# Performance work log

Hardware: AMD Instinct MI355X
Metric: run time of the kernel (lower is better)

The kernel has to match this reference:

```python
import jax, jax.numpy as jnp
import numpy as np

BS, T, H = 4, 2048, 512
N_HEAD = 8
D_HEAD = H // N_HEAD  # 64


def setup_inputs() -> dict:
    key = jax.random.key(0)
    k1, k2, k3 = jax.random.split(key, 3)
    x = jax.random.normal(k1, (BS, T, H), dtype=jnp.float32)
    # torch Linear(hidden, (2*n_head+1)*d_head) -> store transposed for x @ W
    w_qkv = jax.random.normal(k2, (H, (2 * N_HEAD + 1) * D_HEAD), dtype=jnp.float32) * (H ** -0.5)
    w_out = jax.random.normal(k3, (D_HEAD, H), dtype=jnp.float32) * (D_HEAD ** -0.5)
    return {"x": x, "w_qkv": w_qkv, "w_out": w_out}


def reference(x, w_qkv, w_out):
    bs, t, h = x.shape
    n_head, d_head = N_HEAD, D_HEAD
    scale = d_head ** -0.5

    qkv = x @ w_qkv  # [bs, t, (2*n_head+1)*d_head]
    q, k, v = jnp.split(qkv, [n_head * d_head, 2 * n_head * d_head], axis=-1)
    q = q.reshape(bs, t, n_head, d_head)
    k = k.reshape(bs, t, n_head, d_head)
    # v stays [bs, t, d_head]: a single V shared across all heads

    # causal mask: -inf strictly above the diagonal
    mask = jnp.triu(jnp.full((t, t), -jnp.inf, dtype=x.dtype), 1)

    # scores: [bs, n_head, t_q, t_k]
    attn_score = jnp.einsum('bqhd,bkhd->bhqk', q, k) * scale + mask
    attn_prob = jax.nn.softmax(attn_score, axis=-1)

    # shared V broadcast over heads: [bs, n_head, t, d_head]
    attn_vec = jnp.einsum('bhqk,bkd->bhqd', attn_prob, v)
    m_attn_vec = jnp.mean(attn_vec, axis=1)  # mean over heads -> [bs, t, d_head]

    out = m_attn_vec @ w_out  # [bs, t, hidden]
    return out, attn_prob
```

## Files before the change

### kernel.cpp

```cpp
#include <hip/hip_runtime.h>

typedef unsigned short u16;
typedef __bf16 bf16x8 __attribute__((ext_vector_type(8)));
typedef float f32x4 __attribute__((ext_vector_type(4)));
static_assert(sizeof(bf16x8) == 16, "bf16x8 must be 16B");

#define MFMA(a, b, c) __builtin_amdgcn_mfma_f32_16x16x32_bf16(a, b, c, 0, 0, 0)

__device__ __forceinline__ u16 f2bf(float f) {
  unsigned u = __float_as_uint(f);
  u += 0x7fffu + ((u >> 16) & 1u);
  return (u16)(u >> 16);
}

__global__ __launch_bounds__(256) void prep_kernel(
    const float* __restrict__ x, const float* __restrict__ wqkv,
    const float* __restrict__ wout, u16* __restrict__ xh,
    u16* __restrict__ wt, u16* __restrict__ wot) {
  int blk = blockIdx.x, tid = threadIdx.x;
  if (blk < 4096) {
    int idx = (blk * 256 + tid) * 4;
    float4 v = *(const float4*)(x + idx);
    ushort4 o;
    o.x = f2bf(v.x); o.y = f2bf(v.y); o.z = f2bf(v.z); o.w = f2bf(v.w);
    *(ushort4*)(xh + idx) = o;
  } else if (blk < 4096 + 2176) {
    int idx = (blk - 4096) * 256 + tid;
    int n = idx >> 9, k = idx & 511;
    float v = wqkv[k * 1088 + n];
    if (n < 512) v *= 0.125f;
    wt[idx] = f2bf(v);
  } else {
    int idx = (blk - 6272) * 256 + tid;
    int n = idx >> 6, d = idx & 63;
    wot[idx] = f2bf(wout[d * 512 + n]);
  }
}

__global__ __launch_bounds__(256) void qkv_gemm_kernel(
    const u16* __restrict__ xh, const u16* __restrict__ wt,
    u16* __restrict__ Qb, u16* __restrict__ Kb, u16* __restrict__ Vt) {
  __shared__ u16 As[128][40];
  __shared__ u16 Bs[64][40];
  const int tid = threadIdx.x;
  const int w = tid >> 6, l = tid & 63, g = l >> 4, c16 = l & 15;
  const int n0 = blockIdx.x * 64;
  const int m0 = blockIdx.y * 128;
  const int arow = tid >> 1, acol = (tid & 1) << 4;
  const int brow = tid >> 2, bcol = (tid & 3) << 3;
  const u16* ap = xh + (size_t)(m0 + arow) * 512 + acol;
  const u16* bp = wt + (size_t)(n0 + brow) * 512 + bcol;
  uint4 pa0 = *(const uint4*)(ap);
  uint4 pa1 = *(const uint4*)(ap + 8);
  uint4 pb0 = *(const uint4*)(bp);
  f32x4 acc[2][4] = {};
  for (int k0 = 0; k0 < 512; k0 += 32) {
    __syncthreads();
    *(uint4*)&As[arow][acol] = pa0;
    *(uint4*)&As[arow][acol + 8] = pa1;
    *(uint4*)&Bs[brow][bcol] = pb0;
    __syncthreads();
    if (k0 + 32 < 512) {
      pa0 = *(const uint4*)(ap + k0 + 32);
      pa1 = *(const uint4*)(ap + k0 + 40);
      pb0 = *(const uint4*)(bp + k0 + 32);
    }
#pragma unroll
    for (int mt = 0; mt < 2; ++mt) {
      bf16x8 a = *(const bf16x8*)&As[w * 32 + mt * 16 + c16][g * 8];
#pragma unroll
      for (int nt = 0; nt < 4; ++nt) {
        bf16x8 b = *(const bf16x8*)&Bs[nt * 16 + c16][g * 8];
        acc[mt][nt] = MFMA(a, b, acc[mt][nt]);
      }
    }
  }
#pragma unroll
  for (int mt = 0; mt < 2; ++mt)
#pragma unroll
    for (int nt = 0; nt < 4; ++nt)
#pragma unroll
      for (int j = 0; j < 4; ++j) {
        u16 bv = f2bf(acc[mt][nt][j]);
        int row = m0 + w * 32 + mt * 16 + g * 4 + j;
        int b = row >> 11, t = row & 2047;
        int col = n0 + nt * 16 + c16;
        if (col < 512) {
          int h = col >> 6, d = col & 63;
          Qb[((size_t)((b << 3) + h) * 2048 + t) * 64 + d] = bv;
        } else if (col < 1024) {
          int cc = col - 512, h = cc >> 6, d = cc & 63;
          Kb[((size_t)((b << 3) + h) * 2048 + t) * 64 + d] = bv;
        } else {
          int d = col - 1024;
          Vt[((size_t)((b << 6) + d)) * 2048 + t] = bv;
        }
      }
}

__global__ __launch_bounds__(256) void attn_kernel(
    const u16* __restrict__ Qb, const u16* __restrict__ Kb,
    const u16* __restrict__ Vt, float* __restrict__ P,
    float* __restrict__ Obuf) {
  __shared__ u16 QP[64][72];
  __shared__ u16 Ks[64][72];
  __shared__ u16 Vs[64][72];
  const int tid = threadIdx.x;
  const int w = tid >> 6, l = tid & 63, g = l >> 4, c16 = l & 15;
  const int bidx = blockIdx.x;
  const int qt = bidx & 31, bh = bidx >> 5, b = bh >> 3;
  const int srow = tid >> 2, scol = (tid & 3) << 4;

  {
    const u16* src = Qb + ((size_t)(bh * 2048 + qt * 64 + srow)) * 64 + scol;
    *(uint4*)&QP[srow][scol] = *(const uint4*)(src);
    *(uint4*)&QP[srow][scol + 8] = *(const uint4*)(src + 8);
  }
  __syncthreads();
  const bf16x8 aq0 = *(const bf16x8*)&QP[w * 16 + c16][g * 8];
  const bf16x8 aq1 = *(const bf16x8*)&QP[w * 16 + c16][32 + g * 8];

  const u16* kbase = Kb + ((size_t)bh * 2048) * 64;
  const u16* vbase = Vt + ((size_t)(b << 6)) * 2048;

  float lsum[4] = {0.f, 0.f, 0.f, 0.f};

  uint4 ka0 = *(const uint4*)(kbase + (size_t)srow * 64 + scol);
  uint4 ka1 = *(const uint4*)(kbase + (size_t)srow * 64 + scol + 8);
  for (int kt = 0; kt <= qt; ++kt) {
    __syncthreads();
    *(uint4*)&Ks[srow][scol] = ka0;
    *(uint4*)&Ks[srow][scol + 8] = ka1;
    __syncthreads();
    if (kt < qt) {
      const u16* knext = kbase + (size_t)((kt + 1) * 64 + srow) * 64 + scol;
      ka0 = *(const uint4*)(knext);
      ka1 = *(const uint4*)(knext + 8);
    }
    float s[4][4];
#pragma unroll
    for (int nt = 0; nt < 4; ++nt) {
      bf16x8 bk0 = *(const bf16x8*)&Ks[nt * 16 + c16][g * 8];
      bf16x8 bk1 = *(const bf16x8*)&Ks[nt * 16 + c16][32 + g * 8];
      f32x4 a = {};
      a = MFMA(aq0, bk0, a);
      a = MFMA(aq1, bk1, a);
#pragma unroll
      for (int j = 0; j < 4; ++j) s[nt][j] = a[j];
    }
    if (kt == qt) {
#pragma unroll
      for (int nt = 0; nt < 4; ++nt)
#pragma unroll
        for (int j = 0; j < 4; ++j)
          if (nt * 16 + c16 > w * 16 + g * 4 + j) s[nt][j] = -3.0e38f;
    }
#pragma unroll
    for (int j = 0; j < 4; ++j)
      lsum[j] += __expf(s[0][j]) + __expf(s[1][j]) +
                 __expf(s[2][j]) + __expf(s[3][j]);
  }
  float rl[4];
#pragma unroll
  for (int j = 0; j < 4; ++j) {
#pragma unroll
    for (int dd = 1; dd < 16; dd <<= 1)
      lsum[j] += __shfl_xor(lsum[j], dd, 64);
    rl[j] = 1.0f / lsum[j];
  }

  f32x4 oacc[4] = {};
  ka0 = *(const uint4*)(kbase + (size_t)srow * 64 + scol);
  ka1 = *(const uint4*)(kbase + (size_t)srow * 64 + scol + 8);
  uint4 va0 = *(const uint4*)(vbase + (size_t)srow * 2048 + scol);
  uint4 va1 = *(const uint4*)(vbase + (size_t)srow * 2048 + scol + 8);
  for (int kt = 0; kt <= qt; ++kt) {
    __syncthreads();
    *(uint4*)&Ks[srow][scol] = ka0;
    *(uint4*)&Ks[srow][scol + 8] = ka1;
    *(uint4*)&Vs[srow][scol] = va0;
    *(uint4*)&Vs[srow][scol + 8] = va1;
    __syncthreads();
    if (kt < qt) {
      const u16* knext = kbase + (size_t)((kt + 1) * 64 + srow) * 64 + scol;
      ka0 = *(const uint4*)(knext);
      ka1 = *(const uint4*)(knext + 8);
      const u16* vnext = vbase + (size_t)srow * 2048 + (kt + 1) * 64 + scol;
      va0 = *(const uint4*)(vnext);
      va1 = *(const uint4*)(vnext + 8);
    }
    float s[4][4];
#pragma unroll
    for (int nt = 0; nt < 4; ++nt) {
      bf16x8 bk0 = *(const bf16x8*)&Ks[nt * 16 + c16][g * 8];
      bf16x8 bk1 = *(const bf16x8*)&Ks[nt * 16 + c16][32 + g * 8];
      f32x4 a = {};
      a = MFMA(aq0, bk0, a);
      a = MFMA(aq1, bk1, a);
#pragma unroll
      for (int j = 0; j < 4; ++j) s[nt][j] = a[j];
    }
    if (kt == qt) {
#pragma unroll
      for (int nt = 0; nt < 4; ++nt)
#pragma unroll
        for (int j = 0; j < 4; ++j)
          if (nt * 16 + c16 > w * 16 + g * 4 + j) s[nt][j] = -3.0e38f;
    }
    float* prow =
        P + ((size_t)(bh * 2048 + qt * 64 + w * 16)) * 2048 + (size_t)kt * 64;
#pragma unroll
    for (int nt = 0; nt < 4; ++nt)
#pragma unroll
      for (int j = 0; j < 4; ++j) {
        float p = __expf(s[nt][j]) * rl[j];
        __builtin_nontemporal_store(
            p, prow + (size_t)(g * 4 + j) * 2048 + nt * 16 + c16);
        QP[w * 16 + g * 4 + j][nt * 16 + c16] = f2bf(p);
      }
    bf16x8 ap0 = *(const bf16x8*)&QP[w * 16 + c16][g * 8];
    bf16x8 ap1 = *(const bf16x8*)&QP[w * 16 + c16][32 + g * 8];
#pragma unroll
    for (int nt = 0; nt < 4; ++nt) {
      bf16x8 bv0 = *(const bf16x8*)&Vs[nt * 16 + c16][g * 8];
      bf16x8 bv1 = *(const bf16x8*)&Vs[nt * 16 + c16][32 + g * 8];
      oacc[nt] = MFMA(ap0, bv0, oacc[nt]);
      oacc[nt] = MFMA(ap1, bv1, oacc[nt]);
    }
  }

  {
    float* obase = Obuf + ((size_t)(bh * 2048 + qt * 64 + w * 16)) * 64;
#pragma unroll
    for (int nt = 0; nt < 4; ++nt)
#pragma unroll
      for (int j = 0; j < 4; ++j)
        obase[(g * 4 + j) * 64 + nt * 16 + c16] = oacc[nt][j];
  }
  {
    int colstart = (qt + 1) * 64;
    int nf4 = (2048 - colstart) >> 2;
    float* base = P + ((size_t)(bh * 2048 + qt * 64)) * 2048;
    f32x4 z = {0.f, 0.f, 0.f, 0.f};
    for (int r = 0; r < 64; ++r) {
      f32x4* rowp = (f32x4*)(base + (size_t)r * 2048 + colstart);
      for (int u = tid; u < nf4; u += 256)
        __builtin_nontemporal_store(z, rowp + u);
    }
  }
}

__global__ __launch_bounds__(256) void mean_kernel(
    const float* __restrict__ Obuf, u16* __restrict__ meanb) {
  int o4 = blockIdx.x * 256 + threadIdx.x;
  int d4 = o4 & 15, t = (o4 >> 4) & 2047, b = o4 >> 15;
  f32x4 acc = {0.f, 0.f, 0.f, 0.f};
#pragma unroll
  for (int h = 0; h < 8; ++h) {
    f32x4 v = *(const f32x4*)(Obuf +
        ((size_t)((b << 3) + h) * 2048 + t) * 64 + d4 * 4);
    acc += v;
  }
  ushort4 o;
  o.x = f2bf(acc[0] * 0.125f); o.y = f2bf(acc[1] * 0.125f);
  o.z = f2bf(acc[2] * 0.125f); o.w = f2bf(acc[3] * 0.125f);
  *(ushort4*)(meanb + (size_t)o4 * 4) = o;
}

__global__ __launch_bounds__(256) void out_gemm_kernel(
    const u16* __restrict__ meanb, const u16* __restrict__ wot,
    float* __restrict__ out) {
  __shared__ u16 As[64][72];
  __shared__ u16 Bs[64][72];
  const int tid = threadIdx.x;
  const int w = tid >> 6, l = tid & 63, g = l >> 4, c16 = l & 15;
  const int n0 = blockIdx.x * 64;
  const int m0 = blockIdx.y * 64;
  const int srow = tid >> 2, scol = (tid & 3) << 4;
  {
    const u16* asrc = meanb + (size_t)(m0 + srow) * 64 + scol;
    *(uint4*)&As[srow][scol] = *(const uint4*)(asrc);
    *(uint4*)&As[srow][scol + 8] = *(const uint4*)(asrc + 8);
    const u16* bsrc = wot + (size_t)(n0 + srow) * 64 + scol;
    *(uint4*)&Bs[srow][scol] = *(const uint4*)(bsrc);
    *(uint4*)&Bs[srow][scol + 8] = *(const uint4*)(bsrc + 8);
  }
  __syncthreads();
  bf16x8 a0 = *(const bf16x8*)&As[w * 16 + c16][g * 8];
  bf16x8 a1 = *(const bf16x8*)&As[w * 16 + c16][32 + g * 8];
  f32x4 acc[4] = {};
#pragma unroll
  for (int nt = 0; nt < 4; ++nt) {
    bf16x8 b0 = *(const bf16x8*)&Bs[nt * 16 + c16][g * 8];
    bf16x8 b1 = *(const bf16x8*)&Bs[nt * 16 + c16][32 + g * 8];
    acc[nt] = MFMA(a0, b0, acc[nt]);
    acc[nt] = MFMA(a1, b1, acc[nt]);
  }
#pragma unroll
  for (int nt = 0; nt < 4; ++nt)
#pragma unroll
    for (int j = 0; j < 4; ++j)
      __builtin_nontemporal_store(
          acc[nt][j],
          out + (size_t)(m0 + w * 16 + g * 4 + j) * 512 + n0 + nt * 16 + c16);
}

extern "C" void kernel_launch(void* const* d_in, const int* in_sizes, int n_in,
                              void* d_out, int out_size, void* d_ws,
                              size_t ws_size, hipStream_t stream) {
  (void)in_sizes; (void)n_in; (void)out_size; (void)ws_size;
  const float* x = (const float*)d_in[0];
  const float* wqkv = (const float*)d_in[1];
  const float* wout = (const float*)d_in[2];
  float* out = (float*)d_out;
  float* P = out + 4194304;

  u16* xh = (u16*)d_ws;
  u16* wt = xh + 4194304;
  u16* wot = wt + 557056;
  u16* Qb = wot + 32768;
  u16* Kb = Qb + 4194304;
  u16* Vt = Kb + 4194304;
  float* Obuf = (float*)(Vt + 524288);
  u16* meanb = xh;

  hipLaunchKernelGGL(prep_kernel, dim3(6400), dim3(256), 0, stream,
                     x, wqkv, wout, xh, wt, wot);
  hipLaunchKernelGGL(qkv_gemm_kernel, dim3(17, 64), dim3(256), 0, stream,
                     xh, wt, Qb, Kb, Vt);
  hipLaunchKernelGGL(attn_kernel, dim3(1024), dim3(256), 0, stream,
                     Qb, Kb, Vt, P, Obuf);
  hipLaunchKernelGGL(mean_kernel, dim3(512), dim3(256), 0, stream,
                     Obuf, meanb);
  hipLaunchKernelGGL(out_gemm_kernel, dim3(8, 128), dim3(256), 0, stream,
                     meanb, wot, out);
}
```

Baseline: 673.7 us.

## Transpose score MFMA for row-contiguous P stores and balance causal block order

Swaps the MFMA operands so each lane holds four consecutive key columns of one query row, and writes P as 16-byte vector nontemporal stores instead of scalar ones. The row-sum reduction simplifies to two shuffles, and bf16 conversion uses the hardware packed-convert instruction. Block-to-query-tile mapping is reversed for alternate head groups to spread causal work across the grid, and s_setprio is raised around the MFMA sections. The intent is to cut P write overhead, which dominates this kernel, at the risk of different LDS write bank patterns for the P tile.

```diff
diff --git a/kernel.cpp b/kernel.cpp
--- a/kernel.cpp
+++ b/kernel.cpp
@@ -108,7 +108,9 @@
   const int tid = threadIdx.x;
   const int w = tid >> 6, l = tid & 63, g = l >> 4, c16 = l & 15;
   const int bidx = blockIdx.x;
-  const int qt = bidx & 31, bh = bidx >> 5, b = bh >> 3;
+  const int ii = bidx >> 5, jj = bidx & 31;
+  const int qt = ((ii >> 3) & 1) ? (31 - jj) : jj;
+  const int bh = ii, b = bh >> 3;
   const int srow = tid >> 2, scol = (tid & 3) << 4;
 
   {
@@ -123,7 +125,7 @@
   const u16* kbase = Kb + ((size_t)bh * 2048) * 64;
   const u16* vbase = Vt + ((size_t)(b << 6)) * 2048;
 
-  float lsum[4] = {0.f, 0.f, 0.f, 0.f};
+  float lsum = 0.f;
 
   uint4 ka0 = *(const uint4*)(kbase + (size_t)srow * 64 + scol);
   uint4 ka1 = *(const uint4*)(kbase + (size_t)srow * 64 + scol + 8);
@@ -137,43 +139,41 @@
       ka0 = *(const uint4*)(knext);
       ka1 = *(const uint4*)(knext + 8);
     }
-    float s[4][4];
+    f32x4 st[4];
+    __builtin_amdgcn_s_setprio(1);
 #pragma unroll
     for (int nt = 0; nt < 4; ++nt) {
-      bf16x8 bk0 = *(const bf16x8*)&Ks[nt * 16 + c16][g * 8];
-      bf16x8 bk1 = *(const bf16x8*)&Ks[nt * 16 + c16][32 + g * 8];
+      bf16x8 k0 = *(const bf16x8*)&Ks[nt * 16 + c16][g * 8];
+      bf16x8 k1 = *(const bf16x8*)&Ks[nt * 16 + c16][32 + g * 8];
       f32x4 a = {};
-      a = MFMA(aq0, bk0, a);
-      a = MFMA(aq1, bk1, a);
-#pragma unroll
-      for (int j = 0; j < 4; ++j) s[nt][j] = a[j];
-    }
+      a = MFMA(k0, aq0, a);
+      a = MFMA(k1, aq1, a);
+      st[nt] = a;
+    }
+    __builtin_amdgcn_s_setprio(0);
     if (kt == qt) {
 #pragma unroll
       for (int nt = 0; nt < 4; ++nt)
 #pragma unroll
         for (int j = 0; j < 4; ++j)
-          if (nt * 16 + c16 > w * 16 + g * 4 + j) s[nt][j] = -3.0e38f;
-    }
-#pragma unroll
-    for (int j = 0; j < 4; ++j)
-      lsum[j] += __expf(s[0][j]) + __expf(s[1][j]) +
-                 __expf(s[2][j]) + __expf(s[3][j]);
-  }
-  float rl[4];
-#pragma unroll
-  for (int j = 0; j < 4; ++j) {
-#pragma unroll
-    for (int dd = 1; dd < 16; dd <<= 1)
-      lsum[j] += __shfl_xor(lsum[j], dd, 64);
-    rl[j] = 1.0f / lsum[j];
-  }
+          if (nt * 16 + g * 4 + j > w * 16 + c16) st[nt][j] = -3.0e38f;
+    }
+#pragma unroll
+    for (int nt = 0; nt < 4; ++nt)
+#pragma unroll
+      for (int j = 0; j < 4; ++j) lsum += __expf(st[nt][j]);
+  }
+  lsum += __shfl_xor(lsum, 16, 64);
+  lsum += __shfl_xor(lsum, 32, 64);
+  const float rl = 1.0f / lsum;
 
   f32x4 oacc[4] = {};
   ka0 = *(const uint4*)(kbase + (size_t)srow * 64 + scol);
   ka1 = *(const uint4*)(kbase + (size_t)srow * 64 + scol + 8);
   uint4 va0 = *(const uint4*)(vbase + (size_t)srow * 2048 + scol);
   uint4 va1 = *(const uint4*)(vbase + (size_t)srow * 2048 + scol + 8);
+  float* prow = P +
+      ((size_t)(bh * 2048 + qt * 64 + w * 16 + c16)) * 2048 + g * 4;
   for (int kt = 0; kt <= qt; ++kt) {
     __syncthreads();
     *(uint4*)&Ks[srow][scol] = ka0;
@@ -189,37 +189,41 @@
       va0 = *(const uint4*)(vnext);
       va1 = *(const uint4*)(vnext + 8);
     }
-    float s[4][4];
+    f32x4 st[4];
+    __builtin_amdgcn_s_setprio(1);
 #pragma unroll
     for (int nt = 0; nt < 4; ++nt) {
-      bf16x8 bk0 = *(const bf16x8*)&Ks[nt * 16 + c16][g * 8];
-      bf16x8 bk1 = *(const bf16x8*)&Ks[nt * 16 + c16][32 + g * 8];
+      bf16x8 k0 = *(const bf16x8*)&Ks[nt * 16 + c16][g * 8];
+      bf16x8 k1 = *(const bf16x8*)&Ks[nt * 16 + c16][32 + g * 8];
       f32x4 a = {};
-      a = MFMA(aq0, bk0, a);
-      a = MFMA(aq1, bk1, a);
-#pragma unroll
-      for (int j = 0; j < 4; ++j) s[nt][j] = a[j];
-    }
+      a = MFMA(k0, aq0, a);
+      a = MFMA(k1, aq1, a);
+      st[nt] = a;
+    }
+    __builtin_amdgcn_s_setprio(0);
     if (kt == qt) {
 #pragma unroll
       for (int nt = 0; nt < 4; ++nt)
 #pragma unroll
         for (int j = 0; j < 4; ++j)
-          if (nt * 16 + c16 > w * 16 + g * 4 + j) s[nt][j] = -3.0e38f;
-    }
-    float* prow =
-        P + ((size_t)(bh * 2048 + qt * 64 + w * 16)) * 2048 + (size_t)kt * 64;
-#pragma unroll
-    for (int nt = 0; nt < 4; ++nt)
-#pragma unroll
-      for (int j = 0; j < 4; ++j) {
-        float p = __expf(s[nt][j]) * rl[j];
-        __builtin_nontemporal_store(
-            p, prow + (size_t)(g * 4 + j) * 2048 + nt * 16 + c16);
-        QP[w * 16 + g * 4 + j][nt * 16 + c16] = f2bf(p);
-      }
+          if (nt * 16 + g * 4 + j > w * 16 + c16) st[nt][j] = -3.0e38f;
+    }
+#pragma unroll
+    for (int nt = 0; nt < 4; ++nt) {
+      f32x4 pv;
+#pragma unroll
+      for (int j = 0; j < 4; ++j) pv[j] = __expf(st[nt][j]) * rl;
+      __builtin_nontemporal_store(
+          pv, (f32x4*)(prow + (size_t)kt * 64 + nt * 16));
+      unsigned r0, r1;
+      asm("v_cvt_pk_bf16_f32 %0, %1, %2" : "=v"(r0) : "v"(pv[0]), "v"(pv[1]));
+      asm("v_cvt_pk_bf16_f32 %0, %1, %2" : "=v"(r1) : "v"(pv[2]), "v"(pv[3]));
+      uint2 pk; pk.x = r0; pk.y = r1;
+      *(uint2*)&QP[w * 16 + c16][nt * 16 + g * 4] = pk;
+    }
     bf16x8 ap0 = *(const bf16x8*)&QP[w * 16 + c16][g * 8];
     bf16x8 ap1 = *(const bf16x8*)&QP[w * 16 + c16][32 + g * 8];
+    __builtin_amdgcn_s_setprio(1);
 #pragma unroll
     for (int nt = 0; nt < 4; ++nt) {
       bf16x8 bv0 = *(const bf16x8*)&Vs[nt * 16 + c16][g * 8];
@@ -227,6 +231,7 @@
       oacc[nt] = MFMA(ap0, bv0, oacc[nt]);
       oacc[nt] = MFMA(ap1, bv1, oacc[nt]);
     }
+    __builtin_amdgcn_s_setprio(0);
   }
 
   {
```

Result: no change. 665.6 us (-1.2%).
